# Kernel tuning notes

Measured on AMD Instinct MI355X. Metric: run time of the kernel, lower is better.

Reference implementation:

```python
import jax, jax.numpy as jnp
import numpy as np

N, K, F, H, C = 16384, 16, 3, 64, 10


def setup_inputs() -> dict:
    key = jax.random.key(0)
    ks = jax.random.split(key, 6)
    pos = jax.random.normal(ks[0], (N, F), jnp.float32)
    batch = jnp.zeros((N,), jnp.int32)  # single graph
    W1 = jax.random.normal(ks[1], (2 * F, H), jnp.float32) * 0.1
    b1 = jnp.zeros((H,), jnp.float32)
    W2 = jax.random.normal(ks[2], (2 * H, H), jnp.float32) * 0.1
    b2 = jnp.zeros((H,), jnp.float32)
    Wc = jax.random.normal(ks[3], (H, C), jnp.float32) * 0.1
    bc = jnp.zeros((C,), jnp.float32)
    return {"pos": pos, "batch": batch, "W1": W1, "b1": b1,
            "W2": W2, "b2": b2, "Wc": Wc, "bc": bc}


def knn_graph(pos, k):
    # brute-force knn with self-loops (loop=True): self has distance 0
    sq = jnp.sum(pos * pos, axis=1)
    d = sq[:, None] + sq[None, :] - 2.0 * (pos @ pos.T)  # [N, N]
    _, idx = jax.lax.top_k(-d, k)  # [N, k] nearest neighbor indices (incl. self)
    return idx


def edge_conv(x, idx, W, b):
    # message for edge j->i: Linear(concat(x_i, x_j - x_i)); aggregate by max over neighbors
    n, k = idx.shape
    xi = x[:, None, :]               # [N, 1, F]
    xj = x[idx]                      # [N, k, F]
    msg = jnp.concatenate([jnp.broadcast_to(xi, (n, k, x.shape[1])), xj - xi], axis=-1)
    m = msg @ W + b                  # [N, k, H]
    return jnp.max(m, axis=1)        # [N, H]


def reference(pos, batch, W1, b1, W2, b2, Wc, bc):
    idx = knn_graph(pos, K)
    h = jax.nn.relu(edge_conv(pos, idx, W1, b1))
    h = jax.nn.relu(edge_conv(h, idx, W2, b2))
    g = jax.ops.segment_max(h, batch, num_segments=1)  # global max pool -> [1, H]
    return g @ Wc + bc
```

## Files before the change

### kernel.cpp

```cpp
#include <hip/hip_runtime.h>

#define NPTS 16384
#define KNN 16
#define HID 64
#define NCLS 10

#define WPB 4
#define QPB 8
#define CPW (NPTS / WPB)
#define SCAP 128

__device__ __forceinline__ float distm2(float qx, float qy, float qz, float4 c) {
    return fmaf(qx, c.x, fmaf(qy, c.y, fmaf(qz, c.z, c.w)));
}

__device__ __forceinline__ unsigned long long dkey(float v, int j) {
    unsigned u = __float_as_uint(v);
    u = (u & 0x80000000u) ? ~u : (u | 0x80000000u);
    return ((unsigned long long)u << 32) | (unsigned)j;
}

__device__ __forceinline__ unsigned long long shfl_xor_u64(unsigned long long x, int m) {
    unsigned hi = (unsigned)__shfl_xor((int)(x >> 32), m, 64);
    unsigned lo = (unsigned)__shfl_xor((int)(x & 0xffffffffu), m, 64);
    return ((unsigned long long)hi << 32) | lo;
}

__device__ __forceinline__ void wave_top16_16(unsigned long long (&key)[16], int lane,
                                              int q, int* __restrict__ idx) {
    int outj = 0x7fffffff;
    for (int r = 0; r < 16; ++r) {
        unsigned long long gm = key[0];
#pragma unroll
        for (int s = 1; s < 16; ++s) gm = key[s] < gm ? key[s] : gm;
#pragma unroll
        for (int st = 1; st < 64; st <<= 1) {
            unsigned long long o = shfl_xor_u64(gm, st);
            gm = o < gm ? o : gm;
        }
        if (lane == r) outj = (int)(gm & 0xffffffffu);
#pragma unroll
        for (int s = 0; s < 16; ++s)
            if (key[s] == gm) key[s] = ~0ull;
    }
    if (lane < 16) idx[q * KNN + lane] = outj;
}

__global__ void prep_kernel(const float* __restrict__ pos, float4* __restrict__ pos4,
                            float4* __restrict__ pm2) {
    int i = blockIdx.x * 256 + threadIdx.x;
    if (i < NPTS) {
        float x = pos[3 * i], y = pos[3 * i + 1], z = pos[3 * i + 2];
        float sq = fmaf(x, x, fmaf(y, y, z * z));
        pos4[i] = make_float4(x, y, z, sq);
        pm2[i] = make_float4(-2.f * x, -2.f * y, -2.f * z, sq);
    }
}

__global__ __launch_bounds__(256) void knn_kernel(const float4* __restrict__ pos4,
                                                  const float4* __restrict__ pm2,
                                                  int* __restrict__ idx) {
    __shared__ unsigned long long keys[QPB][SCAP];
    __shared__ int knt[QPB];
    __shared__ float smin[QPB][WPB][16];
    int tid = threadIdx.x;
    int lane = tid & 63;
    int w = tid >> 6;
    int qb = blockIdx.x * QPB;
    float qx[QPB], qy[QPB], qz[QPB];
#pragma unroll
    for (int i = 0; i < QPB; ++i) {
        float4 t = pos4[qb + i];
        qx[i] = t.x; qy[i] = t.y; qz[i] = t.z;
    }
    int base = w * CPW;

    float mn[QPB];
#pragma unroll
    for (int i = 0; i < QPB; ++i) mn[i] = INFINITY;
    {
        float4 c0 = pm2[base + lane],       c1 = pm2[base + 64 + lane];
        float4 d0 = pm2[base + 128 + lane], d1 = pm2[base + 192 + lane];
        for (int cb = base; cb < base + CPW; cb += 128) {
#pragma unroll
            for (int i = 0; i < QPB; ++i) mn[i] = fminf(mn[i], distm2(qx[i], qy[i], qz[i], c0));
#pragma unroll
            for (int i = 0; i < QPB; ++i) mn[i] = fminf(mn[i], distm2(qx[i], qy[i], qz[i], c1));
            c0 = d0; c1 = d1;
            d0 = pm2[cb + 256 + lane];
            d1 = pm2[cb + 320 + lane];
        }
    }
#pragma unroll
    for (int i = 0; i < QPB; ++i) {
        float m = mn[i];
        m = fminf(m, __shfl_xor(m, 16, 64));
        m = fminf(m, __shfl_xor(m, 32, 64));
        if (lane < 16) smin[i][w][lane] = m;
    }
    if (tid < QPB) knt[tid] = 0;
    __syncthreads();

    float tq[QPB];
#pragma unroll
    for (int i = 0; i < QPB; ++i) {
        int s = lane & 15;
        float m = fminf(fminf(smin[i][0][s], smin[i][1][s]),
                        fminf(smin[i][2][s], smin[i][3][s]));
        m = fmaxf(m, __shfl_xor(m, 1, 64));
        m = fmaxf(m, __shfl_xor(m, 2, 64));
        m = fmaxf(m, __shfl_xor(m, 4, 64));
        m = fmaxf(m, __shfl_xor(m, 8, 64));
        tq[i] = m;
    }

    {
        float4 c0 = pm2[base + lane],       c1 = pm2[base + 64 + lane];
        float4 d0 = pm2[base + 128 + lane], d1 = pm2[base + 192 + lane];
        for (int cb = base; cb < base + CPW; cb += 128) {
            int j0 = cb + lane, j1 = cb + 64 + lane;
#pragma unroll
            for (int i = 0; i < QPB; ++i) {
                float va = distm2(qx[i], qy[i], qz[i], c0);
                float vb = distm2(qx[i], qy[i], qz[i], c1);
                if (fminf(va, vb) <= tq[i]) {
                    if (va <= tq[i]) { int s = atomicAdd(&knt[i], 1); if (s < SCAP) keys[i][s] = dkey(va, j0); }
                    if (vb <= tq[i]) { int s = atomicAdd(&knt[i], 1); if (s < SCAP) keys[i][s] = dkey(vb, j1); }
                }
            }
            c0 = d0; c1 = d1;
            d0 = pm2[cb + 256 + lane];
            d1 = pm2[cb + 320 + lane];
        }
    }
    __syncthreads();

#pragma unroll
    for (int e = 0; e < 2; ++e) {
        int qi = w * 2 + e;
        int q = qb + qi;
        int ntot = knt[qi];
        if (ntot <= SCAP) {
            unsigned long long k0 = (lane < ntot) ? keys[qi][lane] : ~0ull;
            unsigned long long k1 = (lane + 64 < ntot) ? keys[qi][lane + 64] : ~0ull;
            int r0 = 0, r1 = 0;
            for (int t = 0; t < ntot; ++t) {
                unsigned long long k = keys[qi][t];
                r0 += (int)(k < k0);
                r1 += (int)(k < k1);
            }
            if (lane < ntot && r0 < KNN) idx[q * KNN + r0] = (int)(k0 & 0xffffffffu);
            if (lane + 64 < ntot && r1 < KNN) idx[q * KNN + r1] = (int)(k1 & 0xffffffffu);
        } else {
            float tqq = tq[qi];
            unsigned long long key[16];
#pragma unroll
            for (int u = 0; u < 16; ++u) key[u] = ~0ull;
            for (int j = lane; j < NPTS; j += 64) {
                float v = distm2(qx[qi], qy[qi], qz[qi], pm2[j]);
                unsigned long long k = dkey(v, j);
                if (v <= tqq && k < key[15]) {
#pragma unroll
                    for (int s = 0; s < 16; ++s) {
                        unsigned long long a = k < key[s] ? k : key[s];
                        unsigned long long b = k < key[s] ? key[s] : k;
                        key[s] = a;
                        k = b;
                    }
                }
            }
            wave_top16_16(key, lane, q, idx);
        }
    }
}

__global__ __launch_bounds__(256) void ec12_kernel(const float4* __restrict__ pos4,
                                                   const int* __restrict__ idx,
                                                   const float* __restrict__ W1,
                                                   const float* __restrict__ b1,
                                                   const float* __restrict__ W2,
                                                   const float* __restrict__ b2,
                                                   float* __restrict__ C2,
                                                   float* __restrict__ Y2) {
    __shared__ float h1s[16][64];
    int t = threadIdx.x & 63;
    int w = threadIdx.x >> 6;
    int pb = blockIdx.x * 16 + w * 4;
    float w0 = W1[0 * HID + t], w1 = W1[1 * HID + t], w2 = W1[2 * HID + t];
    float v0 = W1[3 * HID + t], v1 = W1[4 * HID + t], v2 = W1[5 * HID + t];
    float bt1 = b1[t];
#pragma unroll
    for (int i = 0; i < 4; ++i) {
        int p = pb + i;
        float4 xi = pos4[p];
        float C = bt1 + xi.x * (w0 - v0) + xi.y * (w1 - v1) + xi.z * (w2 - v2);
        float m = -INFINITY;
#pragma unroll
        for (int k = 0; k < KNN; ++k) {
            int j = idx[p * KNN + k];
            float4 xj = pos4[j];
            m = fmaxf(m, fmaf(xj.x, v0, fmaf(xj.y, v1, xj.z * v2)));
        }
        h1s[w * 4 + i][t] = fmaxf(C + m, 0.f);
    }
    __syncthreads();
    float aa[4] = {0.f, 0.f, 0.f, 0.f};
    float ab[4] = {0.f, 0.f, 0.f, 0.f};
#pragma unroll 8
    for (int f = 0; f < 64; ++f) {
        float wa = W2[f * HID + t];
        float wb = W2[(64 + f) * HID + t];
#pragma unroll
        for (int i = 0; i < 4; ++i) {
            float h = h1s[w * 4 + i][f];
            aa[i] = fmaf(h, wa, aa[i]);
            ab[i] = fmaf(h, wb, ab[i]);
        }
    }
    float bt = b2[t];
#pragma unroll
    for (int i = 0; i < 4; ++i) {
        C2[(pb + i) * HID + t] = bt + aa[i] - ab[i];
        Y2[(pb + i) * HID + t] = ab[i];
    }
}

__global__ __launch_bounds__(256) void ec2_maxpool_kernel(const float* __restrict__ C2,
                                                          const float* __restrict__ Y2,
                                                          const int* __restrict__ idx,
                                                          float* __restrict__ gpartial) {
    int t = threadIdx.x & 63;
    int lp = threadIdx.x >> 6;
    int p = blockIdx.x * 4 + lp;
    float m = -INFINITY;
#pragma unroll
    for (int k = 0; k < KNN; ++k) {
        int j = idx[p * KNN + k];
        m = fmaxf(m, Y2[j * HID + t]);
    }
    float val = fmaxf(C2[p * HID + t] + m, 0.f);
    __shared__ float red[4][64];
    red[lp][t] = val;
    __syncthreads();
    if (lp == 0) {
        float g = fmaxf(fmaxf(red[0][t], red[1][t]), fmaxf(red[2][t], red[3][t]));
        gpartial[blockIdx.x * 64 + t] = g;
    }
}

__global__ __launch_bounds__(256) void greduce2_kernel(const float* __restrict__ gpartial,
                                                       float* __restrict__ gp2) {
    __shared__ float red[4][64];
    int f = threadIdx.x & 63;
    int w = threadIdx.x >> 6;
    int r0 = blockIdx.x * 16 + w * 4;
    float m = -INFINITY;
#pragma unroll
    for (int r = 0; r < 4; ++r) m = fmaxf(m, gpartial[(r0 + r) * 64 + f]);
    red[w][f] = m;
    __syncthreads();
    if (w == 0)
        gp2[blockIdx.x * 64 + f] =
            fmaxf(fmaxf(red[0][f], red[1][f]), fmaxf(red[2][f], red[3][f]));
}

__global__ __launch_bounds__(256) void tail2_kernel(const float* __restrict__ gp2,
                                                    const float* __restrict__ Wc,
                                                    const float* __restrict__ bc,
                                                    float* __restrict__ out) {
    __shared__ float red[4][64];
    __shared__ float g[64];
    int f = threadIdx.x & 63;
    int w = threadIdx.x >> 6;
    float m = -INFINITY;
    for (int i = w; i < 256; i += 4) m = fmaxf(m, gp2[i * 64 + f]);
    red[w][f] = m;
    __syncthreads();
    if (w == 0) g[f] = fmaxf(fmaxf(red[0][f], red[1][f]), fmaxf(red[2][f], red[3][f]));
    __syncthreads();
    if (threadIdx.x < NCLS) {
        float a = bc[threadIdx.x];
#pragma unroll
        for (int h = 0; h < HID; ++h) a = fmaf(g[h], Wc[h * NCLS + threadIdx.x], a);
        out[threadIdx.x] = a;
    }
}

extern "C" void kernel_launch(void* const* d_in, const int* in_sizes, int n_in,
                              void* d_out, int out_size, void* d_ws, size_t ws_size,
                              hipStream_t stream) {
    const float* pos = (const float*)d_in[0];
    const float* W1 = (const float*)d_in[2];
    const float* b1 = (const float*)d_in[3];
    const float* W2 = (const float*)d_in[4];
    const float* b2 = (const float*)d_in[5];
    const float* Wc = (const float*)d_in[6];
    const float* bc = (const float*)d_in[7];
    float* out = (float*)d_out;

    char* ws = (char*)d_ws;
    size_t o = 0;
    auto alloc = [&](size_t bytes) { size_t r = o; o += (bytes + 255) & ~size_t(255); return r; };
    size_t fm = (size_t)NPTS * HID * 4;
    size_t o_pos4 = alloc((size_t)NPTS * 16);
    size_t o_pm2 = alloc((size_t)(NPTS + 320) * 16);
    size_t o_idx = alloc((size_t)NPTS * KNN * 4);
    size_t o_C2 = alloc(fm);
    size_t o_Y2 = alloc(fm);
    size_t o_gp = alloc((size_t)(NPTS / 4) * HID * 4);
    size_t o_gp2 = alloc((size_t)256 * HID * 4);

    float4* pos4 = (float4*)(ws + o_pos4);
    float4* pm2 = (float4*)(ws + o_pm2);
    int* idx = (int*)(ws + o_idx);
    float* C2 = (float*)(ws + o_C2);
    float* Y2 = (float*)(ws + o_Y2);
    float* gp = (float*)(ws + o_gp);
    float* gp2 = (float*)(ws + o_gp2);

    hipMemsetAsync(pm2 + NPTS, 0, 320 * sizeof(float4), stream);

    prep_kernel<<<NPTS / 256, 256, 0, stream>>>(pos, pos4, pm2);
    knn_kernel<<<NPTS / QPB, 256, 0, stream>>>(pos4, pm2, idx);
    ec12_kernel<<<NPTS / 16, 256, 0, stream>>>(pos4, idx, W1, b1, W2, b2, C2, Y2);
    ec2_maxpool_kernel<<<NPTS / 4, 256, 0, stream>>>(C2, Y2, idx, gp);
    greduce2_kernel<<<256, 256, 0, stream>>>(gp, gp2);
    tail2_kernel<<<1, 256, 0, stream>>>(gp2, Wc, bc, out);
}
```

Before: 306.2 us.

## Replace brute-force kNN scan with uniform grid spatial binning

Bins points into a 32^3 uniform grid using a histogram, a single-block prefix scan and a scatter into cell-sorted order. Each wave handles four spatially adjacent sorted queries: it estimates a distance threshold from nearby cells, then scans only the cells within that radius, collecting candidates into shared memory. Queries whose candidate list overflows or comes up short fall back to a brute-force wave scan. This removes the O(N^2) all-pairs distance work but adds three small kernels, including a serial single-block scan, and depends on the points being roughly evenly distributed.

Result: slower. 1.005 ms (+228.3%).

```diff
diff --git a/kernel.cpp b/kernel.cpp
--- a/kernel.cpp
+++ b/kernel.cpp
@@ -5,9 +5,11 @@
 #define HID 64
 #define NCLS 10
 
-#define WPB 4
-#define QPB 8
-#define CPW (NPTS / WPB)
+#define GRID 32
+#define GRID3 (GRID * GRID * GRID)
+#define GLO -4.2f
+#define GH 0.2625f
+#define INVH (1.0f / GH)
 #define SCAP 128
 
 __device__ __forceinline__ float distm2(float qx, float qy, float qz, float4 c) {
@@ -26,8 +28,26 @@
     return ((unsigned long long)hi << 32) | lo;
 }
 
-__device__ __forceinline__ void wave_top16_16(unsigned long long (&key)[16], int lane,
-                                              int q, int* __restrict__ idx) {
+__device__ void wave_brute16(float qx, float qy, float qz, float tqq,
+                             const float4* __restrict__ spm2,
+                             const int* __restrict__ sid,
+                             int lane, int qorig, int* __restrict__ idx) {
+    unsigned long long key[16];
+#pragma unroll
+    for (int u = 0; u < 16; ++u) key[u] = ~0ull;
+    for (int j = lane; j < NPTS; j += 64) {
+        float v = distm2(qx, qy, qz, spm2[j]);
+        unsigned long long k = dkey(v, sid[j]);
+        if (v <= tqq && k < key[15]) {
+#pragma unroll
+            for (int s = 0; s < 16; ++s) {
+                unsigned long long a = k < key[s] ? k : key[s];
+                unsigned long long b = k < key[s] ? key[s] : k;
+                key[s] = a;
+                k = b;
+            }
+        }
+    }
     int outj = 0x7fffffff;
     for (int r = 0; r < 16; ++r) {
         unsigned long long gm = key[0];
@@ -43,70 +63,123 @@
         for (int s = 0; s < 16; ++s)
             if (key[s] == gm) key[s] = ~0ull;
     }
-    if (lane < 16) idx[q * KNN + lane] = outj;
+    if (lane < 16) idx[qorig * KNN + lane] = outj;
+}
+
+__device__ __forceinline__ int cellof(float x) {
+    int c = (int)floorf((x - GLO) * INVH);
+    return min(max(c, 0), GRID - 1);
 }
 
 __global__ void prep_kernel(const float* __restrict__ pos, float4* __restrict__ pos4,
-                            float4* __restrict__ pm2) {
+                            float4* __restrict__ pm2, int* __restrict__ cellid,
+                            int* __restrict__ hist) {
     int i = blockIdx.x * 256 + threadIdx.x;
     if (i < NPTS) {
         float x = pos[3 * i], y = pos[3 * i + 1], z = pos[3 * i + 2];
         float sq = fmaf(x, x, fmaf(y, y, z * z));
         pos4[i] = make_float4(x, y, z, sq);
         pm2[i] = make_float4(-2.f * x, -2.f * y, -2.f * z, sq);
-    }
-}
-
-__global__ __launch_bounds__(256) void knn_kernel(const float4* __restrict__ pos4,
-                                                  const float4* __restrict__ pm2,
+        int c = (cellof(z) * GRID + cellof(y)) * GRID + cellof(x);
+        cellid[i] = c;
+        atomicAdd(&hist[c], 1);
+    }
+}
+
+__global__ __launch_bounds__(1024) void scan_kernel(const int* __restrict__ hist,
+                                                    int* __restrict__ cellstart,
+                                                    int* __restrict__ cursor) {
+    __shared__ int s[1024];
+    int t = threadIdx.x;
+    int base = 0;
+    for (int c = 0; c < GRID3; c += 1024) {
+        int v = hist[c + t];
+        s[t] = v;
+        __syncthreads();
+        for (int off = 1; off < 1024; off <<= 1) {
+            int x = (t >= off) ? s[t - off] : 0;
+            __syncthreads();
+            s[t] += x;
+            __syncthreads();
+        }
+        int excl = base + s[t] - v;
+        cellstart[c + t] = excl;
+        cursor[c + t] = excl;
+        int tot = s[1023];
+        __syncthreads();
+        base += tot;
+    }
+    if (t == 0) cellstart[GRID3] = base;
+}
+
+__global__ void scatter_kernel(const float4* __restrict__ pos4, const float4* __restrict__ pm2,
+                               const int* __restrict__ cellid, int* __restrict__ cursor,
+                               float4* __restrict__ ssp4, float4* __restrict__ spm2,
+                               int* __restrict__ sid) {
+    int i = blockIdx.x * 256 + threadIdx.x;
+    if (i < NPTS) {
+        int dst = atomicAdd(&cursor[cellid[i]], 1);
+        ssp4[dst] = pos4[i];
+        spm2[dst] = pm2[i];
+        sid[dst] = i;
+    }
+}
+
+__global__ __launch_bounds__(256) void knn_kernel(const float4* __restrict__ ssp4,
+                                                  const float4* __restrict__ spm2,
+                                                  const int* __restrict__ sid,
+                                                  const int* __restrict__ cellstart,
                                                   int* __restrict__ idx) {
-    __shared__ unsigned long long keys[QPB][SCAP];
-    __shared__ int knt[QPB];
-    __shared__ float smin[QPB][WPB][16];
+    __shared__ unsigned long long keys[16][SCAP];
+    __shared__ int knt[16];
     int tid = threadIdx.x;
     int lane = tid & 63;
     int w = tid >> 6;
-    int qb = blockIdx.x * QPB;
-    float qx[QPB], qy[QPB], qz[QPB];
-#pragma unroll
-    for (int i = 0; i < QPB; ++i) {
-        float4 t = pos4[qb + i];
+    int sq0 = blockIdx.x * 16 + w * 4;
+    float qx[4], qy[4], qz[4];
+    int qorig[4];
+#pragma unroll
+    for (int i = 0; i < 4; ++i) {
+        float4 t = ssp4[sq0 + i];
         qx[i] = t.x; qy[i] = t.y; qz[i] = t.z;
-    }
-    int base = w * CPW;
-
-    float mn[QPB];
-#pragma unroll
-    for (int i = 0; i < QPB; ++i) mn[i] = INFINITY;
-    {
-        float4 c0 = pm2[base + lane],       c1 = pm2[base + 64 + lane];
-        float4 d0 = pm2[base + 128 + lane], d1 = pm2[base + 192 + lane];
-        for (int cb = base; cb < base + CPW; cb += 128) {
-#pragma unroll
-            for (int i = 0; i < QPB; ++i) mn[i] = fminf(mn[i], distm2(qx[i], qy[i], qz[i], c0));
-#pragma unroll
-            for (int i = 0; i < QPB; ++i) mn[i] = fminf(mn[i], distm2(qx[i], qy[i], qz[i], c1));
-            c0 = d0; c1 = d1;
-            d0 = pm2[cb + 256 + lane];
-            d1 = pm2[cb + 320 + lane];
-        }
-    }
-#pragma unroll
-    for (int i = 0; i < QPB; ++i) {
-        float m = mn[i];
+        qorig[i] = sid[sq0 + i];
+    }
+
+    float tq[4];
+#pragma unroll
+    for (int i = 0; i < 4; ++i) {
+        int cx = cellof(qx[i]), cy = cellof(qy[i]), cz = cellof(qz[i]);
+        int x0 = max(cx - 1, 0), x1 = min(cx + 1, GRID - 1);
+        int y0 = max(cy - 1, 0), y1 = min(cy + 1, GRID - 1);
+        int z0 = max(cz - 1, 0), z1 = min(cz + 1, GRID - 1);
+        int cnt = 0;
+        for (int span = 1; span <= 6; ++span) {
+            cnt = 0;
+            for (int zz = z0; zz <= z1; ++zz)
+                for (int yy = y0; yy <= y1; ++yy) {
+                    int rb = (zz * GRID + yy) * GRID;
+                    cnt += cellstart[rb + x1 + 1] - cellstart[rb + x0];
+                }
+            if (cnt >= 64) break;
+            x0 = max(x0 - 1, 0); x1 = min(x1 + 1, GRID - 1);
+            y0 = max(y0 - 1, 0); y1 = min(y1 + 1, GRID - 1);
+            z0 = max(z0 - 1, 0); z1 = min(z1 + 1, GRID - 1);
+        }
+        if (cnt < 64) { tq[i] = INFINITY; continue; }
+        float mnl = INFINITY;
+        int rem = 256;
+        for (int zz = z0; zz <= z1 && rem > 0; ++zz)
+            for (int yy = y0; yy <= y1 && rem > 0; ++yy) {
+                int rb = (zz * GRID + yy) * GRID;
+                int rs = cellstart[rb + x0], re = cellstart[rb + x1 + 1];
+                for (int ch = rs; ch < re && rem > 0; ch += 64, rem -= 64) {
+                    int j = ch + lane;
+                    if (j < re) mnl = fminf(mnl, distm2(qx[i], qy[i], qz[i], spm2[j]));
+                }
+            }
+        float m = mnl;
         m = fminf(m, __shfl_xor(m, 16, 64));
         m = fminf(m, __shfl_xor(m, 32, 64));
-        if (lane < 16) smin[i][w][lane] = m;
-    }
-    if (tid < QPB) knt[tid] = 0;
-    __syncthreads();
-
-    float tq[QPB];
-#pragma unroll
-    for (int i = 0; i < QPB; ++i) {
-        int s = lane & 15;
-        float m = fminf(fminf(smin[i][0][s], smin[i][1][s]),
-                        fminf(smin[i][2][s], smin[i][3][s]));
         m = fmaxf(m, __shfl_xor(m, 1, 64));
         m = fmaxf(m, __shfl_xor(m, 2, 64));
         m = fmaxf(m, __shfl_xor(m, 4, 64));
@@ -114,63 +187,80 @@
         tq[i] = m;
     }
 
-    {
-        float4 c0 = pm2[base + lane],       c1 = pm2[base + 64 + lane];
-        float4 d0 = pm2[base + 128 + lane], d1 = pm2[base + 192 + lane];
-        for (int cb = base; cb < base + CPW; cb += 128) {
-            int j0 = cb + lane, j1 = cb + 64 + lane;
-#pragma unroll
-            for (int i = 0; i < QPB; ++i) {
-                float va = distm2(qx[i], qy[i], qz[i], c0);
-                float vb = distm2(qx[i], qy[i], qz[i], c1);
-                if (fminf(va, vb) <= tq[i]) {
-                    if (va <= tq[i]) { int s = atomicAdd(&knt[i], 1); if (s < SCAP) keys[i][s] = dkey(va, j0); }
-                    if (vb <= tq[i]) { int s = atomicAdd(&knt[i], 1); if (s < SCAP) keys[i][s] = dkey(vb, j1); }
-                }
-            }
-            c0 = d0; c1 = d1;
-            d0 = pm2[cb + 256 + lane];
-            d1 = pm2[cb + 320 + lane];
-        }
-    }
-    __syncthreads();
-
-#pragma unroll
-    for (int e = 0; e < 2; ++e) {
-        int qi = w * 2 + e;
-        int q = qb + qi;
-        int ntot = knt[qi];
-        if (ntot <= SCAP) {
-            unsigned long long k0 = (lane < ntot) ? keys[qi][lane] : ~0ull;
-            unsigned long long k1 = (lane + 64 < ntot) ? keys[qi][lane + 64] : ~0ull;
-            int r0 = 0, r1 = 0;
-            for (int t = 0; t < ntot; ++t) {
-                unsigned long long k = keys[qi][t];
-                r0 += (int)(k < k0);
-                r1 += (int)(k < k1);
-            }
-            if (lane < ntot && r0 < KNN) idx[q * KNN + r0] = (int)(k0 & 0xffffffffu);
-            if (lane + 64 < ntot && r1 < KNN) idx[q * KNN + r1] = (int)(k1 & 0xffffffffu);
-        } else {
-            float tqq = tq[qi];
-            unsigned long long key[16];
-#pragma unroll
-            for (int u = 0; u < 16; ++u) key[u] = ~0ull;
-            for (int j = lane; j < NPTS; j += 64) {
-                float v = distm2(qx[qi], qy[qi], qz[qi], pm2[j]);
-                unsigned long long k = dkey(v, j);
-                if (v <= tqq && k < key[15]) {
-#pragma unroll
-                    for (int s = 0; s < 16; ++s) {
-                        unsigned long long a = k < key[s] ? k : key[s];
-                        unsigned long long b = k < key[s] ? key[s] : k;
-                        key[s] = a;
-                        k = b;
+    if (lane < 4) knt[w * 4 + lane] = 0;
+    float rmax2 = fmaxf(fmaxf(tq[0], tq[1]), fmaxf(tq[2], tq[3]));
+    float sqq[4];
+#pragma unroll
+    for (int i = 0; i < 4; ++i) sqq[i] = fmaf(qx[i], qx[i], fmaf(qy[i], qy[i], qz[i] * qz[i]));
+    float r2t = fmaxf(fmaxf(tq[0] + sqq[0], tq[1] + sqq[1]),
+                      fmaxf(tq[2] + sqq[2], tq[3] + sqq[3]));
+    bool wavebrute = (rmax2 > 1e37f) || !(r2t >= 0.f);
+    if (!wavebrute) {
+        float r = sqrtf(fmaxf(r2t, 0.f));
+        r = fminf(r, 20.f);
+        float qminx = fminf(fminf(qx[0], qx[1]), fminf(qx[2], qx[3]));
+        float qmaxx = fmaxf(fmaxf(qx[0], qx[1]), fmaxf(qx[2], qx[3]));
+        float qminy = fminf(fminf(qy[0], qy[1]), fminf(qy[2], qy[3]));
+        float qmaxy = fmaxf(fmaxf(qy[0], qy[1]), fmaxf(qy[2], qy[3]));
+        float qminz = fminf(fminf(qz[0], qz[1]), fminf(qz[2], qz[3]));
+        float qmaxz = fmaxf(fmaxf(qz[0], qz[1]), fmaxf(qz[2], qz[3]));
+        int bz0 = cellof(qminz - r), bz1 = cellof(qmaxz + r);
+        int by0 = cellof(qminy - r), by1 = cellof(qmaxy + r);
+        float r2 = r * r;
+        for (int zz = bz0; zz <= bz1; ++zz) {
+            float zlo = GLO + zz * GH, zhi = zlo + GH;
+            float dz = fmaxf(0.f, fmaxf(zlo - qmaxz, qminz - zhi));
+            if (zz == 0) dz = (qminz > zhi) ? dz : 0.f;
+            if (zz == GRID - 1) dz = (qmaxz < zlo) ? dz : 0.f;
+            for (int yy = by0; yy <= by1; ++yy) {
+                float ylo = GLO + yy * GH, yhi = ylo + GH;
+                float dy = fmaxf(0.f, fmaxf(ylo - qmaxy, qminy - yhi));
+                if (yy == 0) dy = (qminy > yhi) ? dy : 0.f;
+                if (yy == GRID - 1) dy = (qmaxy < ylo) ? dy : 0.f;
+                float d2 = dz * dz + dy * dy;
+                if (d2 > r2) continue;
+                float xr = sqrtf(r2 - d2);
+                int xlo = cellof(qminx - xr);
+                int xhi = cellof(qmaxx + xr);
+                int rb = (zz * GRID + yy) * GRID;
+                int rs = cellstart[rb + xlo], re = cellstart[rb + xhi + 1];
+                for (int ch = rs; ch < re; ch += 64) {
+                    int j = ch + lane;
+                    if (j < re) {
+                        float4 c = spm2[j];
+                        int oid = sid[j];
+                        float v0 = distm2(qx[0], qy[0], qz[0], c);
+                        float v1 = distm2(qx[1], qy[1], qz[1], c);
+                        float v2 = distm2(qx[2], qy[2], qz[2], c);
+                        float v3 = distm2(qx[3], qy[3], qz[3], c);
+                        if (v0 <= tq[0]) { int s = atomicAdd(&knt[w * 4 + 0], 1); if (s < SCAP) keys[w * 4 + 0][s] = dkey(v0, oid); }
+                        if (v1 <= tq[1]) { int s = atomicAdd(&knt[w * 4 + 1], 1); if (s < SCAP) keys[w * 4 + 1][s] = dkey(v1, oid); }
+                        if (v2 <= tq[2]) { int s = atomicAdd(&knt[w * 4 + 2], 1); if (s < SCAP) keys[w * 4 + 2][s] = dkey(v2, oid); }
+                        if (v3 <= tq[3]) { int s = atomicAdd(&knt[w * 4 + 3], 1); if (s < SCAP) keys[w * 4 + 3][s] = dkey(v3, oid); }
                     }
                 }
             }
-            wave_top16_16(key, lane, q, idx);
-        }
+        }
+    }
+
+#pragma unroll
+    for (int e = 0; e < 4; ++e) {
+        int li = w * 4 + e;
+        int ntot = knt[li];
+        if (wavebrute || tq[e] > 1e37f || ntot > SCAP || ntot < KNN) {
+            wave_brute16(qx[e], qy[e], qz[e], INFINITY, spm2, sid, lane, qorig[e], idx);
+            continue;
+        }
+        unsigned long long k0 = (lane < ntot) ? keys[li][lane] : ~0ull;
+        unsigned long long k1 = (lane + 64 < ntot) ? keys[li][lane + 64] : ~0ull;
+        int r0 = 0, r1 = 0;
+        for (int t = 0; t < ntot; ++t) {
+            unsigned long long k = keys[li][t];
+            r0 += (int)(k < k0);
+            r1 += (int)(k < k1);
+        }
+        if (lane < ntot && r0 < KNN) idx[qorig[e] * KNN + r0] = (int)(k0 & 0xffffffffu);
+        if (lane + 64 < ntot && r1 < KNN) idx[qorig[e] * KNN + r1] = (int)(k1 & 0xffffffffu);
     }
 }
 
@@ -303,7 +393,14 @@
     auto alloc = [&](size_t bytes) { size_t r = o; o += (bytes + 255) & ~size_t(255); return r; };
     size_t fm = (size_t)NPTS * HID * 4;
     size_t o_pos4 = alloc((size_t)NPTS * 16);
-    size_t o_pm2 = alloc((size_t)(NPTS + 320) * 16);
+    size_t o_pm2 = alloc((size_t)NPTS * 16);
+    size_t o_ssp4 = alloc((size_t)NPTS * 16);
+    size_t o_spm2 = alloc((size_t)NPTS * 16);
+    size_t o_cellid = alloc((size_t)NPTS * 4);
+    size_t o_sid = alloc((size_t)NPTS * 4);
+    size_t o_hist = alloc((size_t)GRID3 * 4);
+    size_t o_cstart = alloc((size_t)(GRID3 + 1) * 4);
+    size_t o_cursor = alloc((size_t)GRID3 * 4);
     size_t o_idx = alloc((size_t)NPTS * KNN * 4);
     size_t o_C2 = alloc(fm);
     size_t o_Y2 = alloc(fm);
@@ -312,16 +409,25 @@
 
     float4* pos4 = (float4*)(ws + o_pos4);
     float4* pm2 = (float4*)(ws + o_pm2);
+    float4* ssp4 = (float4*)(ws + o_ssp4);
+    float4* spm2 = (float4*)(ws + o_spm2);
+    int* cellid = (int*)(ws + o_cellid);
+    int* sid = (int*)(ws + o_sid);
+    int* hist = (int*)(ws + o_hist);
+    int* cstart = (int*)(ws + o_cstart);
+    int* cursor = (int*)(ws + o_cursor);
     int* idx = (int*)(ws + o_idx);
     float* C2 = (float*)(ws + o_C2);
     float* Y2 = (float*)(ws + o_Y2);
     float* gp = (float*)(ws + o_gp);
     float* gp2 = (float*)(ws + o_gp2);
 
-    hipMemsetAsync(pm2 + NPTS, 0, 320 * sizeof(float4), stream);
-
-    prep_kernel<<<NPTS / 256, 256, 0, stream>>>(pos, pos4, pm2);
-    knn_kernel<<<NPTS / QPB, 256, 0, stream>>>(pos4, pm2, idx);
+    hipMemsetAsync(hist, 0, (size_t)GRID3 * 4, stream);
+
+    prep_kernel<<<NPTS / 256, 256, 0, stream>>>(pos, pos4, pm2, cellid, hist);
+    scan_kernel<<<1, 1024, 0, stream>>>(hist, cstart, cursor);
+    scatter_kernel<<<NPTS / 256, 256, 0, stream>>>(pos4, pm2, cellid, cursor, ssp4, spm2, sid);
+    knn_kernel<<<NPTS / 16, 256, 0, stream>>>(ssp4, spm2, sid, cstart, idx);
     ec12_kernel<<<NPTS / 16, 256, 0, stream>>>(pos4, idx, W1, b1, W2, b2, C2, Y2);
     ec2_maxpool_kernel<<<NPTS / 4, 256, 0, stream>>>(C2, Y2, idx, gp);
     greduce2_kernel<<<256, 256, 0, stream>>>(gp, gp2);
```
